# Optimization experiments

Measured on AMD Instinct MI355X. Metric: run time of the kernel, lower is better.

Reference implementation:

```python
import jax, jax.numpy as jnp
import numpy as np

EPS = 1e-5  # torch group_norm default
GROUPS = 32


def _nin(t, W, b):
    # torch Nin: einsum('bchw,co->bowh') transposes spatial dims, then adds bias
    return jnp.einsum('bchw,co->bowh', t, W) + b


def setup_inputs() -> dict:
    key = jax.random.key(0)
    ks = jax.random.split(key, 9)
    B, C, N = 16, 512, 32
    x = jax.random.normal(ks[0], (B, C, N, N), jnp.float32)
    sc = 0.02
    Wq = jax.random.normal(ks[1], (C, C), jnp.float32) * sc
    Wk = jax.random.normal(ks[2], (C, C), jnp.float32) * sc
    Wv = jax.random.normal(ks[3], (C, C), jnp.float32) * sc
    Wn = jax.random.normal(ks[4], (C, C), jnp.float32) * sc
    bq = jnp.zeros((1, C, 1, 1), jnp.float32)
    bk = jnp.zeros((1, C, 1, 1), jnp.float32)
    bv = jnp.zeros((1, C, 1, 1), jnp.float32)
    bn = jnp.zeros((1, C, 1, 1), jnp.float32)
    return {"x": x, "Wq": Wq, "bq": bq, "Wk": Wk, "bk": bk,
            "Wv": Wv, "bv": bv, "Wn": Wn, "bn": bn}


def reference(x, Wq, bq, Wk, bk, Wv, bv, Wn, bn):
    B, C, H, W = x.shape
    # GroupNorm(32) with no affine params
    xg = x.reshape(B, GROUPS, -1)
    mu = xg.mean(-1, keepdims=True)
    var = xg.var(-1, keepdims=True)
    h = ((xg - mu) / jnp.sqrt(var + EPS)).reshape(B, C, H, W)
    # Nin projections -> spatially transposed (B, C, W, H)
    q = _nin(h, Wq, bq)
    k = _nin(h, Wk, bk)
    v = _nin(h, Wv, bv)
    # scores s[b,w1,w2,h1,h2] = sum_c q[b,c,w1,h1] k[b,c,w2,h2] * C^-0.5
    s = jnp.einsum('bcwh,bcWH->bwWhH', q, k) * (C ** -0.5)
    # softmax over flat (h1,h2) blocks exactly as the torch reshape does
    s = jax.nn.softmax(s.reshape(B, H, W, H * W), axis=-1).reshape(B, H, W, H, W)
    # torch.einsum('bHWHW, bcWH -> bcWH', w, v) takes the DIAGONAL over the
    # repeated H and W labels: diag[b,i,j] = s[b,i,j,i,j], then elementwise
    # scales v: out[b,c,w,h] = diag[b,h,w] * v[b,c,w,h]
    i = jnp.arange(H)
    j = jnp.arange(W)
    diag = s[:, i[:, None], j[None, :], i[:, None], j[None, :]]  # (B,H,W)
    h2 = v * jnp.swapaxes(diag, 1, 2)[:, None]  # (B,C,W,H)
    out = _nin(h2, Wn, bn)  # transposes back -> (B,C,H,W)
    return x + out
```

## Files before the change

kernel.cpp:

```cpp
#include <hip/hip_runtime.h>
#include <hip/hip_bf16.h>

typedef __attribute__((ext_vector_type(8))) short short8;
typedef __attribute__((ext_vector_type(4))) float floatx4;

#define MFMA16(a, b, c) __builtin_amdgcn_mfma_f32_16x16x32_bf16((a), (b), (c), 0, 0, 0)

__device__ __forceinline__ short f2bf(float f) {
    union { float f; unsigned u; } x; x.f = f;
    unsigned r = (x.u + 0x7fffu + ((x.u >> 16) & 1u)) >> 16;
    return (short)r;
}

__device__ __forceinline__ void gl2lds16(const short* g, short* l) {
    void* gv = const_cast<short*>(g);
    __builtin_amdgcn_global_load_lds((__attribute__((address_space(1))) void*)gv,
                                     (__attribute__((address_space(3))) void*)l,
                                     16, 0, 0);
}

__global__ void transpose_w4(const float* __restrict__ Wq, const float* __restrict__ Wk,
                             const float* __restrict__ Wv, const float* __restrict__ Wn,
                             const float* __restrict__ bq, const float* __restrict__ bk,
                             const float* __restrict__ bv,
                             short* __restrict__ Wqkv_t, short* __restrict__ Wn_t,
                             float* __restrict__ bias_cat) {
    __shared__ float t[32][33];
    int z = blockIdx.z;
    const float* Wsrc = (z == 0) ? Wq : (z == 1) ? Wk : (z == 2) ? Wv : Wn;
    int o0 = blockIdx.x * 32, c0 = blockIdx.y * 32;
    int lx = threadIdx.x, ly = threadIdx.y;
    for (int i = ly; i < 32; i += 8) t[i][lx] = Wsrc[(size_t)(c0 + i) * 512 + o0 + lx];
    __syncthreads();
    for (int i = ly; i < 32; i += 8) {
        short v = f2bf(t[lx][i]);
        if (z < 3) Wqkv_t[(size_t)(z * 512 + o0 + i) * 512 + c0 + lx] = v;
        else       Wn_t[(size_t)(o0 + i) * 512 + c0 + lx] = v;
    }
    if (z < 3 && blockIdx.y == 0 && ly == 0) {
        const float* bsrc = (z == 0) ? bq : (z == 1) ? bk : bv;
        bias_cat[z * 512 + o0 + lx] = bsrc[o0 + lx];
    }
}

__global__ __launch_bounds__(256) void groupnorm_k(const float* __restrict__ x,
                                                   short* __restrict__ hnt) {
    int b = blockIdx.x >> 5, g = blockIdx.x & 31;
    const float* xg = x + ((size_t)b * 512 + g * 16) * 1024;
    const float4* xg4 = (const float4*)xg;
    float s = 0.f, ss = 0.f;
    for (int i = threadIdx.x; i < 4096; i += 256) {
        float4 v = xg4[i];
        s  += v.x + v.y + v.z + v.w;
        ss += v.x * v.x + v.y * v.y + v.z * v.z + v.w * v.w;
    }
#pragma unroll
    for (int off = 32; off > 0; off >>= 1) {
        s  += __shfl_down(s,  off, 64);
        ss += __shfl_down(ss, off, 64);
    }
    __shared__ float red[8];
    int w = threadIdx.x >> 6;
    if ((threadIdx.x & 63) == 0) { red[w] = s; red[4 + w] = ss; }
    __syncthreads();
    float S  = red[0] + red[1] + red[2] + red[3];
    float SS = red[4] + red[5] + red[6] + red[7];
    float mean = S * (1.f / 16384.f);
    float var  = SS * (1.f / 16384.f) - mean * mean;
    float rstd = rsqrtf(var + 1e-5f);
    __shared__ __attribute__((aligned(16))) short tile[16 * 1026];
    for (int i = threadIdx.x; i < 4096; i += 256) {
        float4 v = xg4[i];
        int c = i >> 8, p = (i & 255) * 4;
        short* tp = tile + c * 1026 + p;
        tp[0] = f2bf((v.x - mean) * rstd);
        tp[1] = f2bf((v.y - mean) * rstd);
        tp[2] = f2bf((v.z - mean) * rstd);
        tp[3] = f2bf((v.w - mean) * rstd);
    }
    __syncthreads();
    for (int i = threadIdx.x; i < 2048; i += 256) {
        int p = i >> 1, half = i & 1;
        short8 v;
#pragma unroll
        for (int j = 0; j < 8; ++j) v[j] = tile[(half * 8 + j) * 1026 + p];
        *(short8*)(hnt + ((size_t)b * 1024 + p) * 512 + g * 16 + half * 8) = v;
    }
}

__global__ __launch_bounds__(256) void qkv_gemm(const short* __restrict__ A,
                                                const short* __restrict__ Wt,
                                                const float* __restrict__ bias_cat,
                                                short* __restrict__ Qp,
                                                short* __restrict__ Kp,
                                                short* __restrict__ Vb) {
    const int tid = threadIdx.x;
    const int wv = tid >> 6, ln = tid & 63;
    const int m0 = blockIdx.x * 128, n0 = blockIdx.y * 128;
    const size_t BS = 1024 * 512;
    const short* Ab = A + (size_t)blockIdx.z * BS;
    const int tsel = n0 >> 9;
    const int permute = (tsel < 2);
    short* Ob = ((tsel == 0) ? Qp : (tsel == 1) ? Kp : Vb) + (size_t)blockIdx.z * BS;

    __shared__ __attribute__((aligned(16))) short As[128 * 32];
    __shared__ __attribute__((aligned(16))) short Bs[128 * 32];

    floatx4 acc[4][4] = {};
    const int wm = (wv >> 1) * 64, wn = (wv & 1) * 64;
    const int fr = ln & 15, fq = ln >> 4;

    for (int kk = 0; kk < 512; kk += 32) {
        __syncthreads();
#pragma unroll
        for (int j = 0; j < 2; ++j) {
            int s = (wv * 2 + j) * 64 + ln;
            int r = s >> 2;
            int q = (s & 3) ^ ((r >> 1) & 3);
            gl2lds16(Ab + (size_t)(m0 + r) * 512 + kk + q * 8, As + (size_t)(wv * 2 + j) * 512);
            gl2lds16(Wt + (size_t)(n0 + r) * 512 + kk + q * 8, Bs + (size_t)(wv * 2 + j) * 512);
        }
        __syncthreads();
        short8 af[4], bfr[4];
#pragma unroll
        for (int t = 0; t < 4; ++t) {
            int ra = wm + t * 16 + fr;
            af[t]  = *(const short8*)(As + ra * 32 + ((fq ^ ((ra >> 1) & 3)) * 8));
            int rb = wn + t * 16 + fr;
            bfr[t] = *(const short8*)(Bs + rb * 32 + ((fq ^ ((rb >> 1) & 3)) * 8));
        }
#pragma unroll
        for (int mt = 0; mt < 4; ++mt)
#pragma unroll
            for (int nt = 0; nt < 4; ++nt)
                acc[mt][nt] = MFMA16(af[mt], bfr[nt], acc[mt][nt]);
    }
#pragma unroll
    for (int mt = 0; mt < 4; ++mt) {
#pragma unroll
        for (int nt = 0; nt < 4; ++nt) {
            int n = n0 + wn + nt * 16 + fr;
            float bvv = bias_cat[n];
            int nn = n & 511;
#pragma unroll
            for (int r = 0; r < 4; ++r) {
                int m = m0 + wm + mt * 16 + fq * 4 + r;
                int mrow = permute ? ((m & 31) * 32 + (m >> 5)) : m;
                Ob[(size_t)mrow * 512 + nn] = f2bf(acc[mt][nt][r] + bvv);
            }
        }
    }
}

__global__ __launch_bounds__(256, 2) void attn_sm(const short* __restrict__ Qp,
                                                  const short* __restrict__ Kp,
                                                  float* __restrict__ Dm) {
    const int tid = threadIdx.x;
    const int wv = tid >> 6, ln = tid & 63;
    const int m0 = blockIdx.x * 128, n0 = blockIdx.y * 256, b = blockIdx.z;
    const short* Qb = Qp + (size_t)b * (1024 * 512);
    const short* Kb = Kp + (size_t)b * (1024 * 512);

    __shared__ __attribute__((aligned(16))) short As[128 * 32];
    __shared__ __attribute__((aligned(16))) short Bs[256 * 32];

    floatx4 acc[4][8] = {};
    const int wm = (wv >> 1) * 64, wn = (wv & 1) * 128;
    const int fr = ln & 15, fq = ln >> 4;

    for (int kk = 0; kk < 512; kk += 32) {
        __syncthreads();
#pragma unroll
        for (int j = 0; j < 2; ++j) {
            int s = (wv * 2 + j) * 64 + ln;
            int r = s >> 2;
            int q = (s & 3) ^ ((r >> 1) & 3);
            gl2lds16(Qb + (size_t)(m0 + r) * 512 + kk + q * 8, As + (size_t)(wv * 2 + j) * 512);
        }
#pragma unroll
        for (int j = 0; j < 4; ++j) {
            int s = (wv * 4 + j) * 64 + ln;
            int r = s >> 2;
            int q = (s & 3) ^ ((r >> 1) & 3);
            gl2lds16(Kb + (size_t)(n0 + r) * 512 + kk + q * 8, Bs + (size_t)(wv * 4 + j) * 512);
        }
        __syncthreads();
        short8 af[4], bfr[8];
#pragma unroll
        for (int t = 0; t < 4; ++t) {
            int ra = wm + t * 16 + fr;
            af[t] = *(const short8*)(As + ra * 32 + ((fq ^ ((ra >> 1) & 3)) * 8));
        }
#pragma unroll
        for (int u = 0; u < 8; ++u) {
            int rb = wn + u * 16 + fr;
            bfr[u] = *(const short8*)(Bs + rb * 32 + ((fq ^ ((rb >> 1) & 3)) * 8));
        }
#pragma unroll
        for (int mt = 0; mt < 4; ++mt)
#pragma unroll
            for (int nt = 0; nt < 8; ++nt)
                acc[mt][nt] = MFMA16(af[mt], bfr[nt], acc[mt][nt]);
    }

    const float scale = 0.04419417382415922f;
    const int wbase = (m0 + wm) >> 5;
    const int Wbase = (n0 + wn) >> 5;
#pragma unroll
    for (int si = 0; si < 2; ++si) {
#pragma unroll
        for (int sj = 0; sj < 4; ++sj) {
            int wg = wbase + si, Wg = Wbase + sj;
            float tv[16];
            float mx = -3.0e38f;
#pragma unroll
            for (int mi = 0; mi < 2; ++mi)
#pragma unroll
                for (int ni = 0; ni < 2; ++ni)
#pragma unroll
                    for (int r = 0; r < 4; ++r) {
                        float u = acc[2 * si + mi][2 * sj + ni][r] * scale;
                        tv[(mi * 2 + ni) * 4 + r] = u;
                        mx = fmaxf(mx, u);
                    }
#pragma unroll
            for (int off = 32; off > 0; off >>= 1) mx = fmaxf(mx, __shfl_xor(mx, off, 64));
            float se = 0.f;
#pragma unroll
            for (int i = 0; i < 16; ++i) se += __expf(tv[i] - mx);
#pragma unroll
            for (int off = 32; off > 0; off >>= 1) se += __shfl_xor(se, off, 64);
            if (fq == ((wg >> 2) & 3) && fr == (Wg & 15)) {
                int mi = wg >> 4, ni = Wg >> 4;
                float numer = tv[(mi * 2 + ni) * 4 + (wg & 3)];
                Dm[((size_t)b * 32 + wg) * 32 + Wg] = __expf(numer - mx) / se;
            }
        }
    }
}

__global__ __launch_bounds__(256) void out_gemm(const short* __restrict__ A,
                                                const short* __restrict__ Wt,
                                                const float* __restrict__ Dm,
                                                const float* __restrict__ bnb,
                                                const float* __restrict__ x,
                                                float* __restrict__ out) {
    const int tid = threadIdx.x;
    const int wv = tid >> 6, ln = tid & 63;
    const int m0 = blockIdx.x * 128, n0 = blockIdx.y * 128, b = blockIdx.z;
    const size_t BS = 1024 * 512;
    const short* Ab = A + (size_t)b * BS;

    __shared__ __attribute__((aligned(16))) short As[128 * 32];
    __shared__ __attribute__((aligned(16))) short Bs[128 * 32];

    floatx4 acc[4][4] = {};
    const int wm = (wv >> 1) * 64, wn = (wv & 1) * 64;
    const int fr = ln & 15, fq = ln >> 4;

    for (int kk = 0; kk < 512; kk += 32) {
        __syncthreads();
#pragma unroll
        for (int j = 0; j < 2; ++j) {
            int s = (wv * 2 + j) * 64 + ln;
            int r = s >> 2;
            int q = (s & 3) ^ ((r >> 1) & 3);
            gl2lds16(Ab + (size_t)(m0 + r) * 512 + kk + q * 8, As + (size_t)(wv * 2 + j) * 512);
            gl2lds16(Wt + (size_t)(n0 + r) * 512 + kk + q * 8, Bs + (size_t)(wv * 2 + j) * 512);
        }
        __syncthreads();
        short8 af[4], bfr[4];
#pragma unroll
        for (int t = 0; t < 4; ++t) {
            int ra = wm + t * 16 + fr;
            af[t]  = *(const short8*)(As + ra * 32 + ((fq ^ ((ra >> 1) & 3)) * 8));
            int rb = wn + t * 16 + fr;
            bfr[t] = *(const short8*)(Bs + rb * 32 + ((fq ^ ((rb >> 1) & 3)) * 8));
        }
#pragma unroll
        for (int mt = 0; mt < 4; ++mt)
#pragma unroll
            for (int nt = 0; nt < 4; ++nt)
                acc[mt][nt] = MFMA16(af[mt], bfr[nt], acc[mt][nt]);
    }
#pragma unroll
    for (int mt = 0; mt < 4; ++mt) {
        int mbase = m0 + wm + mt * 16 + fq * 4;
        float4 d4 = *(const float4*)(Dm + (size_t)b * 1024 + mbase);
#pragma unroll
        for (int nt = 0; nt < 4; ++nt) {
            int n = n0 + wn + nt * 16 + fr;
            float bvv = bnb[n];
            size_t base = ((size_t)b * 512 + n) * 1024 + mbase;
            float4 x4 = *(const float4*)(x + base);
            float4 o;
            o.x = x4.x + d4.x * acc[mt][nt][0] + bvv;
            o.y = x4.y + d4.y * acc[mt][nt][1] + bvv;
            o.z = x4.z + d4.z * acc[mt][nt][2] + bvv;
            o.w = x4.w + d4.w * acc[mt][nt][3] + bvv;
            *(float4*)(out + base) = o;
        }
    }
}

extern "C" void kernel_launch(void* const* d_in, const int* in_sizes, int n_in,
                              void* d_out, int out_size, void* d_ws, size_t ws_size,
                              hipStream_t stream) {
    const float* x  = (const float*)d_in[0];
    const float* Wq = (const float*)d_in[1];
    const float* bq = (const float*)d_in[2];
    const float* Wk = (const float*)d_in[3];
    const float* bk = (const float*)d_in[4];
    const float* Wv = (const float*)d_in[5];
    const float* bv = (const float*)d_in[6];
    const float* Wn = (const float*)d_in[7];
    const float* bn = (const float*)d_in[8];
    float* out = (float*)d_out;
    char* ws = (char*)d_ws;

    const size_t WQKV = (size_t)1536 * 512 * 2;
    const size_t WSZ  = (size_t)512 * 512 * 2;
    const size_t BIAS = 1536 * sizeof(float);
    const size_t TSZ  = (size_t)16 * 1024 * 512 * 2;
    short* Wqkv_t   = (short*)(ws);
    short* Wn_t     = (short*)(ws + WQKV);
    float* bias_cat = (float*)(ws + WQKV + WSZ);
    char*  base     = ws + WQKV + WSZ + BIAS;
    short* hnt = (short*)(base);
    short* Qp  = (short*)(base + TSZ);
    short* Kp  = (short*)(base + 2 * TSZ);
    short* Vb  = (short*)(base + 3 * TSZ);
    float* Dm  = (float*)(base + 4 * TSZ);

    transpose_w4<<<dim3(16, 16, 4), dim3(32, 8), 0, stream>>>(
        Wq, Wk, Wv, Wn, bq, bk, bv, Wqkv_t, Wn_t, bias_cat);
    groupnorm_k<<<512, 256, 0, stream>>>(x, hnt);
    qkv_gemm<<<dim3(8, 12, 16), 256, 0, stream>>>(hnt, Wqkv_t, bias_cat, Qp, Kp, Vb);
    attn_sm<<<dim3(8, 4, 16), 256, 0, stream>>>(Qp, Kp, Dm);
    out_gemm<<<dim3(8, 4, 16), 256, 0, stream>>>(Vb, Wn_t, Dm, bn, x, out);
}
```

Baseline: 209.7 us.

## Double-buffer LDS tiles in all three GEMM kernels to overlap loads with MFMA

```diff
diff --git a/kernel.cpp b/kernel.cpp
--- a/kernel.cpp
+++ b/kernel.cpp
@@ -103,37 +103,53 @@
     const int permute = (tsel < 2);
     short* Ob = ((tsel == 0) ? Qp : (tsel == 1) ? Kp : Vb) + (size_t)blockIdx.z * BS;
 
-    __shared__ __attribute__((aligned(16))) short As[128 * 32];
-    __shared__ __attribute__((aligned(16))) short Bs[128 * 32];
+    __shared__ __attribute__((aligned(16))) short As[2][128 * 32];
+    __shared__ __attribute__((aligned(16))) short Bs[2][128 * 32];
 
     floatx4 acc[4][4] = {};
     const int wm = (wv >> 1) * 64, wn = (wv & 1) * 64;
     const int fr = ln & 15, fq = ln >> 4;
 
+    int sr[2], sq[2];
+#pragma unroll
+    for (int j = 0; j < 2; ++j) {
+        int s = (wv * 2 + j) * 64 + ln;
+        sr[j] = s >> 2;
+        sq[j] = ((s & 3) ^ ((sr[j] >> 1) & 3)) * 8;
+    }
+
+#pragma unroll
+    for (int j = 0; j < 2; ++j) {
+        gl2lds16(Ab + (size_t)(m0 + sr[j]) * 512 + sq[j], &As[0][(wv * 2 + j) * 512]);
+        gl2lds16(Wt + (size_t)(n0 + sr[j]) * 512 + sq[j], &Bs[0][(wv * 2 + j) * 512]);
+    }
+    __syncthreads();
+
+    int cur = 0;
     for (int kk = 0; kk < 512; kk += 32) {
-        __syncthreads();
-#pragma unroll
-        for (int j = 0; j < 2; ++j) {
-            int s = (wv * 2 + j) * 64 + ln;
-            int r = s >> 2;
-            int q = (s & 3) ^ ((r >> 1) & 3);
-            gl2lds16(Ab + (size_t)(m0 + r) * 512 + kk + q * 8, As + (size_t)(wv * 2 + j) * 512);
-            gl2lds16(Wt + (size_t)(n0 + r) * 512 + kk + q * 8, Bs + (size_t)(wv * 2 + j) * 512);
-        }
-        __syncthreads();
+        if (kk < 480) {
+            int nxt = cur ^ 1;
+#pragma unroll
+            for (int j = 0; j < 2; ++j) {
+                gl2lds16(Ab + (size_t)(m0 + sr[j]) * 512 + kk + 32 + sq[j], &As[nxt][(wv * 2 + j) * 512]);
+                gl2lds16(Wt + (size_t)(n0 + sr[j]) * 512 + kk + 32 + sq[j], &Bs[nxt][(wv * 2 + j) * 512]);
+            }
+        }
         short8 af[4], bfr[4];
 #pragma unroll
         for (int t = 0; t < 4; ++t) {
             int ra = wm + t * 16 + fr;
-            af[t]  = *(const short8*)(As + ra * 32 + ((fq ^ ((ra >> 1) & 3)) * 8));
+            af[t]  = *(const short8*)(&As[cur][ra * 32 + ((fq ^ ((ra >> 1) & 3)) * 8)]);
             int rb = wn + t * 16 + fr;
-            bfr[t] = *(const short8*)(Bs + rb * 32 + ((fq ^ ((rb >> 1) & 3)) * 8));
+            bfr[t] = *(const short8*)(&Bs[cur][rb * 32 + ((fq ^ ((rb >> 1) & 3)) * 8)]);
         }
 #pragma unroll
         for (int mt = 0; mt < 4; ++mt)
 #pragma unroll
             for (int nt = 0; nt < 4; ++nt)
                 acc[mt][nt] = MFMA16(af[mt], bfr[nt], acc[mt][nt]);
+        __syncthreads();
+        cur ^= 1;
     }
 #pragma unroll
     for (int mt = 0; mt < 4; ++mt) {
@@ -161,46 +177,64 @@
     const short* Qb = Qp + (size_t)b * (1024 * 512);
     const short* Kb = Kp + (size_t)b * (1024 * 512);
 
-    __shared__ __attribute__((aligned(16))) short As[128 * 32];
-    __shared__ __attribute__((aligned(16))) short Bs[256 * 32];
+    __shared__ __attribute__((aligned(16))) short As[2][128 * 32];
+    __shared__ __attribute__((aligned(16))) short Bs[2][256 * 32];
 
     floatx4 acc[4][8] = {};
     const int wm = (wv >> 1) * 64, wn = (wv & 1) * 128;
     const int fr = ln & 15, fq = ln >> 4;
 
+    int ar[2], aq[2], br[4], bq_[4];
+#pragma unroll
+    for (int j = 0; j < 2; ++j) {
+        int s = (wv * 2 + j) * 64 + ln;
+        ar[j] = s >> 2;
+        aq[j] = ((s & 3) ^ ((ar[j] >> 1) & 3)) * 8;
+    }
+#pragma unroll
+    for (int j = 0; j < 4; ++j) {
+        int s = (wv * 4 + j) * 64 + ln;
+        br[j] = s >> 2;
+        bq_[j] = ((s & 3) ^ ((br[j] >> 1) & 3)) * 8;
+    }
+
+#pragma unroll
+    for (int j = 0; j < 2; ++j)
+        gl2lds16(Qb + (size_t)(m0 + ar[j]) * 512 + aq[j], &As[0][(wv * 2 + j) * 512]);
+#pragma unroll
+    for (int j = 0; j < 4; ++j)
+        gl2lds16(Kb + (size_t)(n0 + br[j]) * 512 + bq_[j], &Bs[0][(wv * 4 + j) * 512]);
+    __syncthreads();
+
+    int cur = 0;
     for (int kk = 0; kk < 512; kk += 32) {
-        __syncthreads();
-#pragma unroll
-        for (int j = 0; j < 2; ++j) {
-            int s = (wv * 2 + j) * 64 + ln;
-            int r = s >> 2;
-            int q = (s & 3) ^ ((r >> 1) & 3);
-            gl2lds16(Qb + (size_t)(m0 + r) * 512 + kk + q * 8, As + (size_t)(wv * 2 + j) * 512);
-        }
-#pragma unroll
-        for (int j = 0; j < 4; ++j) {
-            int s = (wv * 4 + j) * 64 + ln;
-            int r = s >> 2;
-            int q = (s & 3) ^ ((r >> 1) & 3);
-            gl2lds16(Kb + (size_t)(n0 + r) * 512 + kk + q * 8, Bs + (size_t)(wv * 4 + j) * 512);
-        }
-        __syncthreads();
+        if (kk < 480) {
+            int nxt = cur ^ 1;
+#pragma unroll
+            for (int j = 0; j < 2; ++j)
+                gl2lds16(Qb + (size_t)(m0 + ar[j]) * 512 + kk + 32 + aq[j], &As[nxt][(wv * 2 + j) * 512]);
+#pragma unroll
+            for (int j = 0; j < 4; ++j)
+                gl2lds16(Kb + (size_t)(n0 + br[j]) * 512 + kk + 32 + bq_[j], &Bs[nxt][(wv * 4 + j) * 512]);
+        }
         short8 af[4], bfr[8];
 #pragma unroll
         for (int t = 0; t < 4; ++t) {
             int ra = wm + t * 16 + fr;
-            af[t] = *(const short8*)(As + ra * 32 + ((fq ^ ((ra >> 1) & 3)) * 8));
+            af[t] = *(const short8*)(&As[cur][ra * 32 + ((fq ^ ((ra >> 1) & 3)) * 8)]);
         }
 #pragma unroll
         for (int u = 0; u < 8; ++u) {
             int rb = wn + u * 16 + fr;
-            bfr[u] = *(const short8*)(Bs + rb * 32 + ((fq ^ ((rb >> 1) & 3)) * 8));
+            bfr[u] = *(const short8*)(&Bs[cur][rb * 32 + ((fq ^ ((rb >> 1) & 3)) * 8)]);
         }
 #pragma unroll
         for (int mt = 0; mt < 4; ++mt)
 #pragma unroll
             for (int nt = 0; nt < 8; ++nt)
                 acc[mt][nt] = MFMA16(af[mt], bfr[nt], acc[mt][nt]);
+        __syncthreads();
+        cur ^= 1;
     }
 
     const float scale = 0.04419417382415922f;
@@ -251,37 +285,53 @@
     const size_t BS = 1024 * 512;
     const short* Ab = A + (size_t)b * BS;
 
-    __shared__ __attribute__((aligned(16))) short As[128 * 32];
-    __shared__ __attribute__((aligned(16))) short Bs[128 * 32];
+    __shared__ __attribute__((aligned(16))) short As[2][128 * 32];
+    __shared__ __attribute__((aligned(16))) short Bs[2][128 * 32];
 
     floatx4 acc[4][4] = {};
     const int wm = (wv >> 1) * 64, wn = (wv & 1) * 64;
     const int fr = ln & 15, fq = ln >> 4;
 
+    int sr[2], sq[2];
+#pragma unroll
+    for (int j = 0; j < 2; ++j) {
+        int s = (wv * 2 + j) * 64 + ln;
+        sr[j] = s >> 2;
+        sq[j] = ((s & 3) ^ ((sr[j] >> 1) & 3)) * 8;
+    }
+
+#pragma unroll
+    for (int j = 0; j < 2; ++j) {
+        gl2lds16(Ab + (size_t)(m0 + sr[j]) * 512 + sq[j], &As[0][(wv * 2 + j) * 512]);
+        gl2lds16(Wt + (size_t)(n0 + sr[j]) * 512 + sq[j], &Bs[0][(wv * 2 + j) * 512]);
+    }
+    __syncthreads();
+
+    int cur = 0;
     for (int kk = 0; kk < 512; kk += 32) {
-        __syncthreads();
-#pragma unroll
-        for (int j = 0; j < 2; ++j) {
-            int s = (wv * 2 + j) * 64 + ln;
-            int r = s >> 2;
-            int q = (s & 3) ^ ((r >> 1) & 3);
-            gl2lds16(Ab + (size_t)(m0 + r) * 512 + kk + q * 8, As + (size_t)(wv * 2 + j) * 512);
-            gl2lds16(Wt + (size_t)(n0 + r) * 512 + kk + q * 8, Bs + (size_t)(wv * 2 + j) * 512);
-        }
-        __syncthreads();
+        if (kk < 480) {
+            int nxt = cur ^ 1;
+#pragma unroll
+            for (int j = 0; j < 2; ++j) {
+                gl2lds16(Ab + (size_t)(m0 + sr[j]) * 512 + kk + 32 + sq[j], &As[nxt][(wv * 2 + j) * 512]);
+                gl2lds16(Wt + (size_t)(n0 + sr[j]) * 512 + kk + 32 + sq[j], &Bs[nxt][(wv * 2 + j) * 512]);
+            }
+        }
         short8 af[4], bfr[4];
 #pragma unroll
         for (int t = 0; t < 4; ++t) {
             int ra = wm + t * 16 + fr;
-            af[t]  = *(const short8*)(As + ra * 32 + ((fq ^ ((ra >> 1) & 3)) * 8));
+            af[t]  = *(const short8*)(&As[cur][ra * 32 + ((fq ^ ((ra >> 1) & 3)) * 8)]);
             int rb = wn + t * 16 + fr;
-            bfr[t] = *(const short8*)(Bs + rb * 32 + ((fq ^ ((rb >> 1) & 3)) * 8));
+            bfr[t] = *(const short8*)(&Bs[cur][rb * 32 + ((fq ^ ((rb >> 1) & 3)) * 8)]);
         }
 #pragma unroll
         for (int mt = 0; mt < 4; ++mt)
 #pragma unroll
             for (int nt = 0; nt < 4; ++nt)
                 acc[mt][nt] = MFMA16(af[mt], bfr[nt], acc[mt][nt]);
+        __syncthreads();
+        cur ^= 1;
     }
 #pragma unroll
     for (int mt = 0; mt < 4; ++mt) {
```

New measurement: 210.7 us. About the same (+0.5%).

## Use 256x256 double-buffered pipelined GEMM tiles with XCD-aware block mapping

Applied to the files above, without the earlier changes.

```diff
diff --git a/kernel.cpp b/kernel.cpp
--- a/kernel.cpp
+++ b/kernel.cpp
@@ -5,6 +5,8 @@
 typedef __attribute__((ext_vector_type(4))) float floatx4;
 
 #define MFMA16(a, b, c) __builtin_amdgcn_mfma_f32_16x16x32_bf16((a), (b), (c), 0, 0, 0)
+#define WAIT_VM(N) asm volatile("s_waitcnt vmcnt(" #N ")" ::: "memory")
+#define BARM() do { asm volatile("" ::: "memory"); __builtin_amdgcn_s_barrier(); asm volatile("" ::: "memory"); } while (0)
 
 __device__ __forceinline__ short f2bf(float f) {
     union { float f; unsigned u; } x; x.f = f;
@@ -88,128 +90,217 @@
     }
 }
 
-__global__ __launch_bounds__(256) void qkv_gemm(const short* __restrict__ A,
-                                                const short* __restrict__ Wt,
-                                                const float* __restrict__ bias_cat,
-                                                short* __restrict__ Qp,
-                                                short* __restrict__ Kp,
-                                                short* __restrict__ Vb) {
+
+__global__ __launch_bounds__(512, 2) void qkv_gemm256(const short* __restrict__ A,
+                                                      const short* __restrict__ Wt,
+                                                      const float* __restrict__ bias_cat,
+                                                      short* __restrict__ Qp,
+                                                      short* __restrict__ Kp,
+                                                      short* __restrict__ Vb) {
     const int tid = threadIdx.x;
-    const int wv = tid >> 6, ln = tid & 63;
-    const int m0 = blockIdx.x * 128, n0 = blockIdx.y * 128;
-    const size_t BS = 1024 * 512;
-    const short* Ab = A + (size_t)blockIdx.z * BS;
+    const int wid = tid >> 6, ln = tid & 63;
+    const int wrow = wid >> 2, wcol = wid & 3;
+    const int fid = blockIdx.x;
+    const int xcd = fid & 7, s = fid >> 3;
+    const int mt = xcd * 8 + s / 6, nt = s % 6;
+    const int m0 = mt * 256, n0 = nt * 256;
     const int tsel = n0 >> 9;
     const int permute = (tsel < 2);
-    short* Ob = ((tsel == 0) ? Qp : (tsel == 1) ? Kp : Vb) + (size_t)blockIdx.z * BS;
-
-    __shared__ __attribute__((aligned(16))) short As[128 * 32];
-    __shared__ __attribute__((aligned(16))) short Bs[128 * 32];
-
-    floatx4 acc[4][4] = {};
-    const int wm = (wv >> 1) * 64, wn = (wv & 1) * 64;
+    short* Ob = (tsel == 0) ? Qp : (tsel == 1) ? Kp : Vb;
+
+    __shared__ __attribute__((aligned(16))) short Asb[2][256 * 64];
+    __shared__ __attribute__((aligned(16))) short Bsb[2][256 * 64];
+
+    floatx4 acc[8][4] = {};
     const int fr = ln & 15, fq = ln >> 4;
 
-    for (int kk = 0; kk < 512; kk += 32) {
-        __syncthreads();
-#pragma unroll
-        for (int j = 0; j < 2; ++j) {
-            int s = (wv * 2 + j) * 64 + ln;
-            int r = s >> 2;
-            int q = (s & 3) ^ ((r >> 1) & 3);
-            gl2lds16(Ab + (size_t)(m0 + r) * 512 + kk + q * 8, As + (size_t)(wv * 2 + j) * 512);
-            gl2lds16(Wt + (size_t)(n0 + r) * 512 + kk + q * 8, Bs + (size_t)(wv * 2 + j) * 512);
-        }
-        __syncthreads();
-        short8 af[4], bfr[4];
+    const int srow = wid * 8 + (ln >> 3);
+    const int schk = (ln & 7) ^ ((ln >> 3) & 7);
+    const short* gA = A + (size_t)(m0 + srow) * 512 + schk * 8;
+    const short* gB = Wt + (size_t)(n0 + srow) * 512 + schk * 8;
+
+    short* Ac = &Asb[0][0]; short* Bc = &Bsb[0][0];
+    short* An = &Asb[1][0]; short* Bn = &Bsb[1][0];
+
+    auto SA = [&](int j, short* db) { gl2lds16(gA + (size_t)j * 32768, db + j * 4096 + wid * 512); };
+    auto SB = [&](int j, short* db) { gl2lds16(gB + (size_t)j * 32768, db + j * 4096 + wid * 512); };
+    auto LDA = [&](const short* Ap, int mh, int ks, short8* dst) {
 #pragma unroll
         for (int t = 0; t < 4; ++t) {
-            int ra = wm + t * 16 + fr;
-            af[t]  = *(const short8*)(As + ra * 32 + ((fq ^ ((ra >> 1) & 3)) * 8));
-            int rb = wn + t * 16 + fr;
-            bfr[t] = *(const short8*)(Bs + rb * 32 + ((fq ^ ((rb >> 1) & 3)) * 8));
-        }
-#pragma unroll
-        for (int mt = 0; mt < 4; ++mt)
-#pragma unroll
-            for (int nt = 0; nt < 4; ++nt)
-                acc[mt][nt] = MFMA16(af[mt], bfr[nt], acc[mt][nt]);
-    }
-#pragma unroll
-    for (int mt = 0; mt < 4; ++mt) {
-#pragma unroll
-        for (int nt = 0; nt < 4; ++nt) {
-            int n = n0 + wn + nt * 16 + fr;
+            int ra = wrow * 128 + (mh * 4 + t) * 16 + fr;
+            dst[t] = *(const short8*)(Ap + ra * 64 + (((ks << 2) | fq) ^ (fr & 7)) * 8);
+        }
+    };
+    auto LDB = [&](const short* Bp, int ks, short8* dst) {
+#pragma unroll
+        for (int nf = 0; nf < 4; ++nf) {
+            int rb = wcol * 64 + nf * 16 + fr;
+            dst[nf] = *(const short8*)(Bp + rb * 64 + (((ks << 2) | fq) ^ (fr & 7)) * 8);
+        }
+    };
+    auto MM = [&](int mh, const short8* a_, const short8* b_) {
+        __builtin_amdgcn_s_setprio(1);
+#pragma unroll
+        for (int t = 0; t < 4; ++t)
+#pragma unroll
+            for (int nf = 0; nf < 4; ++nf)
+                acc[mh * 4 + t][nf] = MFMA16(a_[t], b_[nf], acc[mh * 4 + t][nf]);
+        __builtin_amdgcn_s_setprio(0);
+    };
+
+    SA(0, Ac); SA(2, Ac); SB(0, Bc); SB(1, Bc); SB(2, Bc); SB(3, Bc); SA(1, Ac); SA(3, Ac);
+    gA += 64; gB += 64;
+    WAIT_VM(2);
+    BARM();
+
+    short8 a_[4], p0[4], p1[4];
+    for (int kt = 0; kt < 8; ++kt) {
+        const bool st = (kt < 7);
+        LDA(Ac, 0, 0, a_); LDB(Bc, 0, p0);
+        if (st) { SA(0, An); SA(2, An); }
+        BARM();
+        MM(0, a_, p0);
+        BARM();
+        LDA(Ac, 0, 1, a_); LDB(Bc, 1, p1);
+        if (st) { SB(0, Bn); SB(1, Bn); }
+        BARM();
+        MM(0, a_, p1);
+        if (st) { WAIT_VM(4); } else { WAIT_VM(0); }
+        BARM();
+        LDA(Ac, 1, 0, a_);
+        if (st) { SB(2, Bn); SB(3, Bn); }
+        BARM();
+        MM(1, a_, p0);
+        BARM();
+        LDA(Ac, 1, 1, a_);
+        if (st) { SA(1, An); SA(3, An); }
+        BARM();
+        MM(1, a_, p1);
+        if (st) { WAIT_VM(2); }
+        BARM();
+        short* t0 = Ac; Ac = An; An = t0;
+        short* t1 = Bc; Bc = Bn; Bn = t1;
+        if (st) { gA += 64; gB += 64; }
+    }
+
+    const size_t BS = 1024 * 512;
+#pragma unroll
+    for (int mf = 0; mf < 8; ++mf) {
+        int m = m0 + wrow * 128 + mf * 16 + fq * 4;
+        int batch = m >> 10;
+        short* Obb = Ob + (size_t)batch * BS;
+#pragma unroll
+        for (int nf = 0; nf < 4; ++nf) {
+            int n = n0 + wcol * 64 + nf * 16 + fr;
             float bvv = bias_cat[n];
             int nn = n & 511;
 #pragma unroll
             for (int r = 0; r < 4; ++r) {
-                int m = m0 + wm + mt * 16 + fq * 4 + r;
-                int mrow = permute ? ((m & 31) * 32 + (m >> 5)) : m;
-                Ob[(size_t)mrow * 512 + nn] = f2bf(acc[mt][nt][r] + bvv);
+                int p = (m + r) & 1023;
+                int mrow = permute ? ((p & 31) * 32 + (p >> 5)) : p;
+                Obb[(size_t)mrow * 512 + nn] = f2bf(acc[mf][nf][r] + bvv);
             }
         }
     }
 }
 
-__global__ __launch_bounds__(256, 2) void attn_sm(const short* __restrict__ Qp,
-                                                  const short* __restrict__ Kp,
-                                                  float* __restrict__ Dm) {
+__global__ __launch_bounds__(512, 2) void attn_sm256(const short* __restrict__ Qp,
+                                                     const short* __restrict__ Kp,
+                                                     float* __restrict__ Dm) {
     const int tid = threadIdx.x;
-    const int wv = tid >> 6, ln = tid & 63;
-    const int m0 = blockIdx.x * 128, n0 = blockIdx.y * 256, b = blockIdx.z;
-    const short* Qb = Qp + (size_t)b * (1024 * 512);
-    const short* Kb = Kp + (size_t)b * (1024 * 512);
-
-    __shared__ __attribute__((aligned(16))) short As[128 * 32];
-    __shared__ __attribute__((aligned(16))) short Bs[256 * 32];
-
-    floatx4 acc[4][8] = {};
-    const int wm = (wv >> 1) * 64, wn = (wv & 1) * 128;
+    const int wid = tid >> 6, ln = tid & 63;
+    const int wrow = wid >> 2, wcol = wid & 3;
+    const int fid = blockIdx.x;
+    const int xcd = fid & 7, slot = fid >> 3;
+    const int b = xcd * 2 + (slot >> 4);
+    const int t4 = slot & 15;
+    const int m0 = (t4 & 3) * 256, n0 = (t4 >> 2) * 256;
+    const size_t BS = 1024 * 512;
+    const short* Qb = Qp + (size_t)b * BS;
+    const short* Kb = Kp + (size_t)b * BS;
+
+    __shared__ __attribute__((aligned(16))) short Asb[2][256 * 64];
+    __shared__ __attribute__((aligned(16))) short Bsb[2][256 * 64];
+
+    floatx4 acc[8][4] = {};
     const int fr = ln & 15, fq = ln >> 4;
 
-    for (int kk = 0; kk < 512; kk += 32) {
-        __syncthreads();
-#pragma unroll
-        for (int j = 0; j < 2; ++j) {
-            int s = (wv * 2 + j) * 64 + ln;
-            int r = s >> 2;
-            int q = (s & 3) ^ ((r >> 1) & 3);
-            gl2lds16(Qb + (size_t)(m0 + r) * 512 + kk + q * 8, As + (size_t)(wv * 2 + j) * 512);
-        }
-#pragma unroll
-        for (int j = 0; j < 4; ++j) {
-            int s = (wv * 4 + j) * 64 + ln;
-            int r = s >> 2;
-            int q = (s & 3) ^ ((r >> 1) & 3);
-            gl2lds16(Kb + (size_t)(n0 + r) * 512 + kk + q * 8, Bs + (size_t)(wv * 4 + j) * 512);
-        }
-        __syncthreads();
-        short8 af[4], bfr[8];
+    const int srow = wid * 8 + (ln >> 3);
+    const int schk = (ln & 7) ^ ((ln >> 3) & 7);
+    const short* gA = Qb + (size_t)(m0 + srow) * 512 + schk * 8;
+    const short* gB = Kb + (size_t)(n0 + srow) * 512 + schk * 8;
+
+    short* Ac = &Asb[0][0]; short* Bc = &Bsb[0][0];
+    short* An = &Asb[1][0]; short* Bn = &Bsb[1][0];
+
+    auto SA = [&](int j, short* db) { gl2lds16(gA + (size_t)j * 32768, db + j * 4096 + wid * 512); };
+    auto SB = [&](int j, short* db) { gl2lds16(gB + (size_t)j * 32768, db + j * 4096 + wid * 512); };
+    auto LDA = [&](const short* Ap, int mh, int ks, short8* dst) {
 #pragma unroll
         for (int t = 0; t < 4; ++t) {
-            int ra = wm + t * 16 + fr;
-            af[t] = *(const short8*)(As + ra * 32 + ((fq ^ ((ra >> 1) & 3)) * 8));
-        }
-#pragma unroll
-        for (int u = 0; u < 8; ++u) {
-            int rb = wn + u * 16 + fr;
-            bfr[u] = *(const short8*)(Bs + rb * 32 + ((fq ^ ((rb >> 1) & 3)) * 8));
-        }
-#pragma unroll
-        for (int mt = 0; mt < 4; ++mt)
-#pragma unroll
-            for (int nt = 0; nt < 8; ++nt)
-                acc[mt][nt] = MFMA16(af[mt], bfr[nt], acc[mt][nt]);
+            int ra = wrow * 128 + (mh * 4 + t) * 16 + fr;
+            dst[t] = *(const short8*)(Ap + ra * 64 + (((ks << 2) | fq) ^ (fr & 7)) * 8);
+        }
+    };
+    auto LDB = [&](const short* Bp, int ks, short8* dst) {
+#pragma unroll
+        for (int nf = 0; nf < 4; ++nf) {
+            int rb = wcol * 64 + nf * 16 + fr;
+            dst[nf] = *(const short8*)(Bp + rb * 64 + (((ks << 2) | fq) ^ (fr & 7)) * 8);
+        }
+    };
+    auto MM = [&](int mh, const short8* a_, const short8* b_) {
+        __builtin_amdgcn_s_setprio(1);
+#pragma unroll
+        for (int t = 0; t < 4; ++t)
+#pragma unroll
+            for (int nf = 0; nf < 4; ++nf)
+                acc[mh * 4 + t][nf] = MFMA16(a_[t], b_[nf], acc[mh * 4 + t][nf]);
+        __builtin_amdgcn_s_setprio(0);
+    };
+
+    SA(0, Ac); SA(2, Ac); SB(0, Bc); SB(1, Bc); SB(2, Bc); SB(3, Bc); SA(1, Ac); SA(3, Ac);
+    gA += 64; gB += 64;
+    WAIT_VM(2);
+    BARM();
+
+    short8 a_[4], p0[4], p1[4];
+    for (int kt = 0; kt < 8; ++kt) {
+        const bool st = (kt < 7);
+        LDA(Ac, 0, 0, a_); LDB(Bc, 0, p0);
+        if (st) { SA(0, An); SA(2, An); }
+        BARM();
+        MM(0, a_, p0);
+        BARM();
+        LDA(Ac, 0, 1, a_); LDB(Bc, 1, p1);
+        if (st) { SB(0, Bn); SB(1, Bn); }
+        BARM();
+        MM(0, a_, p1);
+        if (st) { WAIT_VM(4); } else { WAIT_VM(0); }
+        BARM();
+        LDA(Ac, 1, 0, a_);
+        if (st) { SB(2, Bn); SB(3, Bn); }
+        BARM();
+        MM(1, a_, p0);
+        BARM();
+        LDA(Ac, 1, 1, a_);
+        if (st) { SA(1, An); SA(3, An); }
+        BARM();
+        MM(1, a_, p1);
+        if (st) { WAIT_VM(2); }
+        BARM();
+        short* t0 = Ac; Ac = An; An = t0;
+        short* t1 = Bc; Bc = Bn; Bn = t1;
+        if (st) { gA += 64; gB += 64; }
     }
 
     const float scale = 0.04419417382415922f;
-    const int wbase = (m0 + wm) >> 5;
-    const int Wbase = (n0 + wn) >> 5;
-#pragma unroll
-    for (int si = 0; si < 2; ++si) {
-#pragma unroll
-        for (int sj = 0; sj < 4; ++sj) {
+    const int wbase = (m0 + wrow * 128) >> 5;
+    const int Wbase = (n0 + wcol * 64) >> 5;
+#pragma unroll
+    for (int si = 0; si < 4; ++si) {
+#pragma unroll
+        for (int sj = 0; sj < 2; ++sj) {
             int wg = wbase + si, Wg = Wbase + sj;
             float tv[16];
             float mx = -3.0e38f;
@@ -247,42 +338,82 @@
                                                 float* __restrict__ out) {
     const int tid = threadIdx.x;
     const int wv = tid >> 6, ln = tid & 63;
-    const int m0 = blockIdx.x * 128, n0 = blockIdx.y * 128, b = blockIdx.z;
+    const int fid = blockIdx.x + (blockIdx.y << 3) + blockIdx.z * 32;
+    const int xcd = fid & 7, slot = fid >> 3;
+    const int bb = (slot >= 32) ? 1 : 0;
+    const int w = slot - bb * 32;
+    const int b = xcd * 2 + bb;
+    const int m0 = (w & 7) * 128, n0 = (w >> 3) * 128;
     const size_t BS = 1024 * 512;
     const short* Ab = A + (size_t)b * BS;
 
-    __shared__ __attribute__((aligned(16))) short As[128 * 32];
-    __shared__ __attribute__((aligned(16))) short Bs[128 * 32];
+    __shared__ __attribute__((aligned(16))) short As[3][128 * 32];
+    __shared__ __attribute__((aligned(16))) short Bs[3][128 * 32];
 
     floatx4 acc[4][4] = {};
     const int wm = (wv >> 1) * 64, wn = (wv & 1) * 64;
     const int fr = ln & 15, fq = ln >> 4;
 
-    for (int kk = 0; kk < 512; kk += 32) {
-        __syncthreads();
-#pragma unroll
-        for (int j = 0; j < 2; ++j) {
-            int s = (wv * 2 + j) * 64 + ln;
-            int r = s >> 2;
-            int q = (s & 3) ^ ((r >> 1) & 3);
-            gl2lds16(Ab + (size_t)(m0 + r) * 512 + kk + q * 8, As + (size_t)(wv * 2 + j) * 512);
-            gl2lds16(Wt + (size_t)(n0 + r) * 512 + kk + q * 8, Bs + (size_t)(wv * 2 + j) * 512);
-        }
-        __syncthreads();
+    int sr[2], sq[2];
+#pragma unroll
+    for (int j = 0; j < 2; ++j) {
+        int s = (wv * 2 + j) * 64 + ln;
+        sr[j] = s >> 2;
+        sq[j] = ((s & 3) ^ ((sr[j] >> 1) & 3)) * 8;
+    }
+    int aoff[4], boff[4];
+#pragma unroll
+    for (int t = 0; t < 4; ++t) {
+        int ra = wm + t * 16 + fr;
+        aoff[t] = ra * 32 + ((fq ^ ((ra >> 1) & 3)) * 8);
+        int rb = wn + t * 16 + fr;
+        boff[t] = rb * 32 + ((fq ^ ((rb >> 1) & 3)) * 8);
+    }
+
+    short* a0 = &As[0][0]; short* a1 = &As[1][0]; short* a2 = &As[2][0];
+    short* b0 = &Bs[0][0]; short* b1 = &Bs[1][0]; short* b2 = &Bs[2][0];
+
+#pragma unroll
+    for (int j = 0; j < 2; ++j) {
+        gl2lds16(Ab + (size_t)(m0 + sr[j]) * 512 + sq[j],      a0 + (wv * 2 + j) * 512);
+        gl2lds16(Wt + (size_t)(n0 + sr[j]) * 512 + sq[j],      b0 + (wv * 2 + j) * 512);
+        gl2lds16(Ab + (size_t)(m0 + sr[j]) * 512 + 32 + sq[j], a1 + (wv * 2 + j) * 512);
+        gl2lds16(Wt + (size_t)(n0 + sr[j]) * 512 + 32 + sq[j], b1 + (wv * 2 + j) * 512);
+    }
+
+    auto compute = [&](const short* Ap, const short* Bp) {
         short8 af[4], bfr[4];
 #pragma unroll
         for (int t = 0; t < 4; ++t) {
-            int ra = wm + t * 16 + fr;
-            af[t]  = *(const short8*)(As + ra * 32 + ((fq ^ ((ra >> 1) & 3)) * 8));
-            int rb = wn + t * 16 + fr;
-            bfr[t] = *(const short8*)(Bs + rb * 32 + ((fq ^ ((rb >> 1) & 3)) * 8));
+            af[t]  = *(const short8*)(Ap + aoff[t]);
+            bfr[t] = *(const short8*)(Bp + boff[t]);
         }
 #pragma unroll
         for (int mt = 0; mt < 4; ++mt)
 #pragma unroll
             for (int nt = 0; nt < 4; ++nt)
                 acc[mt][nt] = MFMA16(af[mt], bfr[nt], acc[mt][nt]);
-    }
+    };
+
+    for (int t = 0; t < 14; ++t) {
+        int kp = t * 32 + 64;
+#pragma unroll
+        for (int j = 0; j < 2; ++j) {
+            gl2lds16(Ab + (size_t)(m0 + sr[j]) * 512 + kp + sq[j], a2 + (wv * 2 + j) * 512);
+            gl2lds16(Wt + (size_t)(n0 + sr[j]) * 512 + kp + sq[j], b2 + (wv * 2 + j) * 512);
+        }
+        WAIT_VM(8);
+        BARM();
+        compute(a0, b0);
+        BARM();
+        short* ta = a0; a0 = a1; a1 = a2; a2 = ta;
+        short* tb = b0; b0 = b1; b1 = b2; b2 = tb;
+    }
+    WAIT_VM(4); BARM();
+    compute(a0, b0);
+    WAIT_VM(0); BARM();
+    compute(a1, b1);
+
 #pragma unroll
     for (int mt = 0; mt < 4; ++mt) {
         int mbase = m0 + wm + mt * 16 + fq * 4;
@@ -335,7 +466,7 @@
     transpose_w4<<<dim3(16, 16, 4), dim3(32, 8), 0, stream>>>(
         Wq, Wk, Wv, Wn, bq, bk, bv, Wqkv_t, Wn_t, bias_cat);
     groupnorm_k<<<512, 256, 0, stream>>>(x, hnt);
-    qkv_gemm<<<dim3(8, 12, 16), 256, 0, stream>>>(hnt, Wqkv_t, bias_cat, Qp, Kp, Vb);
-    attn_sm<<<dim3(8, 4, 16), 256, 0, stream>>>(Qp, Kp, Dm);
+    qkv_gemm256<<<384, 512, 0, stream>>>(hnt, Wqkv_t, bias_cat, Qp, Kp, Vb);
+    attn_sm256<<<256, 512, 0, stream>>>(Qp, Kp, Dm);
     out_gemm<<<dim3(8, 4, 16), 256, 0, stream>>>(Vb, Wn_t, Dm, bn, x, out);
 }
```

Result: faster. 199.3 us (-5.0%).

## Restructure GEMMs to stage full-K A tile in LDS and stream B from global

Applied to the files above, without the earlier changes.

```diff
diff --git a/kernel.cpp b/kernel.cpp
--- a/kernel.cpp
+++ b/kernel.cpp
@@ -88,128 +88,146 @@
     }
 }
 
-__global__ __launch_bounds__(256) void qkv_gemm(const short* __restrict__ A,
-                                                const short* __restrict__ Wt,
-                                                const float* __restrict__ bias_cat,
-                                                short* __restrict__ Qp,
-                                                short* __restrict__ Kp,
-                                                short* __restrict__ Vb) {
+
+__global__ __launch_bounds__(512, 2) void qkv_fk(const short* __restrict__ A,
+                                                 const short* __restrict__ Wt,
+                                                 const float* __restrict__ bias_cat,
+                                                 short* __restrict__ Qp,
+                                                 short* __restrict__ Kp,
+                                                 short* __restrict__ Vb) {
     const int tid = threadIdx.x;
-    const int wv = tid >> 6, ln = tid & 63;
-    const int m0 = blockIdx.x * 128, n0 = blockIdx.y * 128;
-    const size_t BS = 1024 * 512;
-    const short* Ab = A + (size_t)blockIdx.z * BS;
+    const int wid = tid >> 6, ln = tid & 63;
+    const int wrow = wid >> 2, wcol = wid & 3;
+    const int fr = ln & 15, fq = ln >> 4, fr7 = fr & 7;
+    const int fid = blockIdx.x;
+    const int xcd = fid & 7, s = fid >> 3;
+    const int m0 = (xcd * 16 + s / 6) * 128, n0 = (s % 6) * 256;
     const int tsel = n0 >> 9;
     const int permute = (tsel < 2);
-    short* Ob = ((tsel == 0) ? Qp : (tsel == 1) ? Kp : Vb) + (size_t)blockIdx.z * BS;
-
-    __shared__ __attribute__((aligned(16))) short As[128 * 32];
-    __shared__ __attribute__((aligned(16))) short Bs[128 * 32];
+    short* Ob = (tsel == 0) ? Qp : (tsel == 1) ? Kp : Vb;
+
+    __shared__ __attribute__((aligned(16))) short Alds[128 * 512];
+
+#pragma unroll
+    for (int j = 0; j < 16; ++j) {
+        int r = wid * 16 + j;
+        gl2lds16(A + (size_t)(m0 + r) * 512 + ((ln ^ (j & 7)) * 8), Alds + r * 512);
+    }
 
     floatx4 acc[4][4] = {};
-    const int wm = (wv >> 1) * 64, wn = (wv & 1) * 64;
-    const int fr = ln & 15, fq = ln >> 4;
-
-    for (int kk = 0; kk < 512; kk += 32) {
-        __syncthreads();
-#pragma unroll
-        for (int j = 0; j < 2; ++j) {
-            int s = (wv * 2 + j) * 64 + ln;
-            int r = s >> 2;
-            int q = (s & 3) ^ ((r >> 1) & 3);
-            gl2lds16(Ab + (size_t)(m0 + r) * 512 + kk + q * 8, As + (size_t)(wv * 2 + j) * 512);
-            gl2lds16(Wt + (size_t)(n0 + r) * 512 + kk + q * 8, Bs + (size_t)(wv * 2 + j) * 512);
-        }
-        __syncthreads();
-        short8 af[4], bfr[4];
-#pragma unroll
-        for (int t = 0; t < 4; ++t) {
-            int ra = wm + t * 16 + fr;
-            af[t]  = *(const short8*)(As + ra * 32 + ((fq ^ ((ra >> 1) & 3)) * 8));
-            int rb = wn + t * 16 + fr;
-            bfr[t] = *(const short8*)(Bs + rb * 32 + ((fq ^ ((rb >> 1) & 3)) * 8));
-        }
-#pragma unroll
-        for (int mt = 0; mt < 4; ++mt)
-#pragma unroll
-            for (int nt = 0; nt < 4; ++nt)
-                acc[mt][nt] = MFMA16(af[mt], bfr[nt], acc[mt][nt]);
-    }
+    const short* lB = Wt + (size_t)(n0 + wcol * 64 + fr) * 512 + fq * 8;
+    const short* lA = Alds + (wrow * 64 + fr) * 512;
+
+    short8 bc[4], bn_[4], af[4];
+#pragma unroll
+    for (int nf = 0; nf < 4; ++nf) bc[nf] = *(const short8*)(lB + nf * 8192);
+
+    __syncthreads();
+
+#pragma unroll
+    for (int t = 0; t < 16; ++t) {
+#pragma unroll
+        for (int mt = 0; mt < 4; ++mt)
+            af[mt] = *(const short8*)(lA + mt * 8192 + ((((t << 2) | fq) ^ fr7) * 8));
+        if (t < 15) {
+#pragma unroll
+            for (int nf = 0; nf < 4; ++nf)
+                bn_[nf] = *(const short8*)(lB + nf * 8192 + t * 32 + 32);
+        }
+#pragma unroll
+        for (int mt = 0; mt < 4; ++mt)
+#pragma unroll
+            for (int nf = 0; nf < 4; ++nf)
+                acc[mt][nf] = MFMA16(af[mt], bc[nf], acc[mt][nf]);
+        if (t < 15) {
+#pragma unroll
+            for (int nf = 0; nf < 4; ++nf) bc[nf] = bn_[nf];
+        }
+    }
+
+    const size_t BS = 1024 * 512;
+    const int batch = m0 >> 10;
+    short* Obb = Ob + (size_t)batch * BS;
 #pragma unroll
     for (int mt = 0; mt < 4; ++mt) {
-#pragma unroll
-        for (int nt = 0; nt < 4; ++nt) {
-            int n = n0 + wn + nt * 16 + fr;
+        int m = m0 + wrow * 64 + mt * 16 + fq * 4;
+#pragma unroll
+        for (int nf = 0; nf < 4; ++nf) {
+            int n = n0 + wcol * 64 + nf * 16 + fr;
             float bvv = bias_cat[n];
             int nn = n & 511;
 #pragma unroll
             for (int r = 0; r < 4; ++r) {
-                int m = m0 + wm + mt * 16 + fq * 4 + r;
-                int mrow = permute ? ((m & 31) * 32 + (m >> 5)) : m;
-                Ob[(size_t)mrow * 512 + nn] = f2bf(acc[mt][nt][r] + bvv);
+                int p = (m + r) & 1023;
+                int mrow = permute ? ((p & 31) * 32 + (p >> 5)) : p;
+                Obb[(size_t)mrow * 512 + nn] = f2bf(acc[mt][nf][r] + bvv);
             }
         }
     }
 }
 
-__global__ __launch_bounds__(256, 2) void attn_sm(const short* __restrict__ Qp,
+__global__ __launch_bounds__(512, 2) void attn_fk(const short* __restrict__ Qp,
                                                   const short* __restrict__ Kp,
                                                   float* __restrict__ Dm) {
     const int tid = threadIdx.x;
-    const int wv = tid >> 6, ln = tid & 63;
-    const int m0 = blockIdx.x * 128, n0 = blockIdx.y * 256, b = blockIdx.z;
-    const short* Qb = Qp + (size_t)b * (1024 * 512);
-    const short* Kb = Kp + (size_t)b * (1024 * 512);
-
-    __shared__ __attribute__((aligned(16))) short As[128 * 32];
-    __shared__ __attribute__((aligned(16))) short Bs[256 * 32];
-
-    floatx4 acc[4][8] = {};
-    const int wm = (wv >> 1) * 64, wn = (wv & 1) * 128;
-    const int fr = ln & 15, fq = ln >> 4;
-
-    for (int kk = 0; kk < 512; kk += 32) {
-        __syncthreads();
-#pragma unroll
-        for (int j = 0; j < 2; ++j) {
-            int s = (wv * 2 + j) * 64 + ln;
-            int r = s >> 2;
-            int q = (s & 3) ^ ((r >> 1) & 3);
-            gl2lds16(Qb + (size_t)(m0 + r) * 512 + kk + q * 8, As + (size_t)(wv * 2 + j) * 512);
-        }
-#pragma unroll
-        for (int j = 0; j < 4; ++j) {
-            int s = (wv * 4 + j) * 64 + ln;
-            int r = s >> 2;
-            int q = (s & 3) ^ ((r >> 1) & 3);
-            gl2lds16(Kb + (size_t)(n0 + r) * 512 + kk + q * 8, Bs + (size_t)(wv * 4 + j) * 512);
-        }
-        __syncthreads();
-        short8 af[4], bfr[8];
-#pragma unroll
-        for (int t = 0; t < 4; ++t) {
-            int ra = wm + t * 16 + fr;
-            af[t] = *(const short8*)(As + ra * 32 + ((fq ^ ((ra >> 1) & 3)) * 8));
-        }
-#pragma unroll
-        for (int u = 0; u < 8; ++u) {
-            int rb = wn + u * 16 + fr;
-            bfr[u] = *(const short8*)(Bs + rb * 32 + ((fq ^ ((rb >> 1) & 3)) * 8));
-        }
-#pragma unroll
-        for (int mt = 0; mt < 4; ++mt)
-#pragma unroll
-            for (int nt = 0; nt < 8; ++nt)
-                acc[mt][nt] = MFMA16(af[mt], bfr[nt], acc[mt][nt]);
+    const int wid = tid >> 6, ln = tid & 63;
+    const int wrow = wid >> 2, wcol = wid & 3;
+    const int fr = ln & 15, fq = ln >> 4, fr7 = fr & 7;
+    const int fid = blockIdx.x;
+    const int xcd = fid & 7, slot = fid >> 3;
+    const int b = xcd * 2 + (slot >> 5);
+    const int inner = slot & 31;
+    const int m0 = (inner & 7) * 128, n0 = (inner >> 3) * 256;
+    const size_t BS = 1024 * 512;
+    const short* Qb = Qp + (size_t)b * BS;
+    const short* Kb = Kp + (size_t)b * BS;
+
+    __shared__ __attribute__((aligned(16))) short Alds[128 * 512];
+
+#pragma unroll
+    for (int j = 0; j < 16; ++j) {
+        int r = wid * 16 + j;
+        gl2lds16(Qb + (size_t)(m0 + r) * 512 + ((ln ^ (j & 7)) * 8), Alds + r * 512);
+    }
+
+    floatx4 acc[4][4] = {};
+    const short* lB = Kb + (size_t)(n0 + wcol * 64 + fr) * 512 + fq * 8;
+    const short* lA = Alds + (wrow * 64 + fr) * 512;
+
+    short8 bc[4], bn_[4], af[4];
+#pragma unroll
+    for (int nf = 0; nf < 4; ++nf) bc[nf] = *(const short8*)(lB + nf * 8192);
+
+    __syncthreads();
+
+#pragma unroll
+    for (int t = 0; t < 16; ++t) {
+#pragma unroll
+        for (int mt = 0; mt < 4; ++mt)
+            af[mt] = *(const short8*)(lA + mt * 8192 + ((((t << 2) | fq) ^ fr7) * 8));
+        if (t < 15) {
+#pragma unroll
+            for (int nf = 0; nf < 4; ++nf)
+                bn_[nf] = *(const short8*)(lB + nf * 8192 + t * 32 + 32);
+        }
+#pragma unroll
+        for (int mt = 0; mt < 4; ++mt)
+#pragma unroll
+            for (int nf = 0; nf < 4; ++nf)
+                acc[mt][nf] = MFMA16(af[mt], bc[nf], acc[mt][nf]);
+        if (t < 15) {
+#pragma unroll
+            for (int nf = 0; nf < 4; ++nf) bc[nf] = bn_[nf];
+        }
     }
 
     const float scale = 0.04419417382415922f;
-    const int wbase = (m0 + wm) >> 5;
-    const int Wbase = (n0 + wn) >> 5;
+    const int wbase = (m0 + wrow * 64) >> 5;
+    const int Wbase = (n0 + wcol * 64) >> 5;
 #pragma unroll
     for (int si = 0; si < 2; ++si) {
 #pragma unroll
-        for (int sj = 0; sj < 4; ++sj) {
+        for (int sj = 0; sj < 2; ++sj) {
             int wg = wbase + si, Wg = Wbase + sj;
             float tv[16];
             float mx = -3.0e38f;
@@ -239,65 +257,78 @@
     }
 }
 
-__global__ __launch_bounds__(256) void out_gemm(const short* __restrict__ A,
-                                                const short* __restrict__ Wt,
-                                                const float* __restrict__ Dm,
-                                                const float* __restrict__ bnb,
-                                                const float* __restrict__ x,
-                                                float* __restrict__ out) {
+__global__ __launch_bounds__(512, 2) void out_fk(const short* __restrict__ A,
+                                                 const short* __restrict__ Wt,
+                                                 const float* __restrict__ Dm,
+                                                 const float* __restrict__ bnb,
+                                                 const float* __restrict__ x,
+                                                 float* __restrict__ out) {
     const int tid = threadIdx.x;
-    const int wv = tid >> 6, ln = tid & 63;
-    const int m0 = blockIdx.x * 128, n0 = blockIdx.y * 128, b = blockIdx.z;
+    const int wid = tid >> 6, ln = tid & 63;
+    const int wrow = wid >> 2, wcol = wid & 3;
+    const int fr = ln & 15, fq = ln >> 4, fr7 = fr & 7;
+    const int fid = blockIdx.x;
+    const int xcd = fid & 7, slot = fid >> 3;
+    const int b = xcd * 2 + (slot >> 4);
+    const int inner = slot & 15;
+    const int m0 = (inner & 7) * 128, n0 = (inner >> 3) * 256;
     const size_t BS = 1024 * 512;
     const short* Ab = A + (size_t)b * BS;
 
-    __shared__ __attribute__((aligned(16))) short As[128 * 32];
-    __shared__ __attribute__((aligned(16))) short Bs[128 * 32];
+    __shared__ __attribute__((aligned(16))) short Alds[128 * 512];
+
+#pragma unroll
+    for (int j = 0; j < 16; ++j) {
+        int r = wid * 16 + j;
+        gl2lds16(Ab + (size_t)(m0 + r) * 512 + ((ln ^ (j & 7)) * 8), Alds + r * 512);
+    }
 
     floatx4 acc[4][4] = {};
-    const int wm = (wv >> 1) * 64, wn = (wv & 1) * 64;
-    const int fr = ln & 15, fq = ln >> 4;
-
-    for (int kk = 0; kk < 512; kk += 32) {
-        __syncthreads();
-#pragma unroll
-        for (int j = 0; j < 2; ++j) {
-            int s = (wv * 2 + j) * 64 + ln;
-            int r = s >> 2;
-            int q = (s & 3) ^ ((r >> 1) & 3);
-            gl2lds16(Ab + (size_t)(m0 + r) * 512 + kk + q * 8, As + (size_t)(wv * 2 + j) * 512);
-            gl2lds16(Wt + (size_t)(n0 + r) * 512 + kk + q * 8, Bs + (size_t)(wv * 2 + j) * 512);
-        }
-        __syncthreads();
-        short8 af[4], bfr[4];
-#pragma unroll
-        for (int t = 0; t < 4; ++t) {
-            int ra = wm + t * 16 + fr;
-            af[t]  = *(const short8*)(As + ra * 32 + ((fq ^ ((ra >> 1) & 3)) * 8));
-            int rb = wn + t * 16 + fr;
-            bfr[t] = *(const short8*)(Bs + rb * 32 + ((fq ^ ((rb >> 1) & 3)) * 8));
-        }
-#pragma unroll
-        for (int mt = 0; mt < 4; ++mt)
-#pragma unroll
-            for (int nt = 0; nt < 4; ++nt)
-                acc[mt][nt] = MFMA16(af[mt], bfr[nt], acc[mt][nt]);
-    }
+    const short* lB = Wt + (size_t)(n0 + wcol * 64 + fr) * 512 + fq * 8;
+    const short* lA = Alds + (wrow * 64 + fr) * 512;
+
+    short8 bc[4], bn_[4], af[4];
+#pragma unroll
+    for (int nf = 0; nf < 4; ++nf) bc[nf] = *(const short8*)(lB + nf * 8192);
+
+    __syncthreads();
+
+#pragma unroll
+    for (int t = 0; t < 16; ++t) {
+#pragma unroll
+        for (int mt = 0; mt < 4; ++mt)
+            af[mt] = *(const short8*)(lA + mt * 8192 + ((((t << 2) | fq) ^ fr7) * 8));
+        if (t < 15) {
+#pragma unroll
+            for (int nf = 0; nf < 4; ++nf)
+                bn_[nf] = *(const short8*)(lB + nf * 8192 + t * 32 + 32);
+        }
+#pragma unroll
+        for (int mt = 0; mt < 4; ++mt)
+#pragma unroll
+            for (int nf = 0; nf < 4; ++nf)
+                acc[mt][nf] = MFMA16(af[mt], bc[nf], acc[mt][nf]);
+        if (t < 15) {
+#pragma unroll
+            for (int nf = 0; nf < 4; ++nf) bc[nf] = bn_[nf];
+        }
+    }
+
 #pragma unroll
     for (int mt = 0; mt < 4; ++mt) {
-        int mbase = m0 + wm + mt * 16 + fq * 4;
+        int mbase = m0 + wrow * 64 + mt * 16 + fq * 4;
         float4 d4 = *(const float4*)(Dm + (size_t)b * 1024 + mbase);
 #pragma unroll
-        for (int nt = 0; nt < 4; ++nt) {
-            int n = n0 + wn + nt * 16 + fr;
+        for (int nf = 0; nf < 4; ++nf) {
+            int n = n0 + wcol * 64 + nf * 16 + fr;
             float bvv = bnb[n];
             size_t base = ((size_t)b * 512 + n) * 1024 + mbase;
             float4 x4 = *(const float4*)(x + base);
             float4 o;
-            o.x = x4.x + d4.x * acc[mt][nt][0] + bvv;
-            o.y = x4.y + d4.y * acc[mt][nt][1] + bvv;
-            o.z = x4.z + d4.z * acc[mt][nt][2] + bvv;
-            o.w = x4.w + d4.w * acc[mt][nt][3] + bvv;
+            o.x = x4.x + d4.x * acc[mt][nf][0] + bvv;
+            o.y = x4.y + d4.y * acc[mt][nf][1] + bvv;
+            o.z = x4.z + d4.z * acc[mt][nf][2] + bvv;
+            o.w = x4.w + d4.w * acc[mt][nf][3] + bvv;
             *(float4*)(out + base) = o;
         }
     }
@@ -335,7 +366,7 @@
     transpose_w4<<<dim3(16, 16, 4), dim3(32, 8), 0, stream>>>(
         Wq, Wk, Wv, Wn, bq, bk, bv, Wqkv_t, Wn_t, bias_cat);
     groupnorm_k<<<512, 256, 0, stream>>>(x, hnt);
-    qkv_gemm<<<dim3(8, 12, 16), 256, 0, stream>>>(hnt, Wqkv_t, bias_cat, Qp, Kp, Vb);
-    attn_sm<<<dim3(8, 4, 16), 256, 0, stream>>>(Qp, Kp, Dm);
-    out_gemm<<<dim3(8, 4, 16), 256, 0, stream>>>(Vb, Wn_t, Dm, bn, x, out);
-}
+    qkv_fk<<<768, 512, 0, stream>>>(hnt, Wqkv_t, bias_cat, Qp, Kp, Vb);
+    attn_fk<<<512, 512, 0, stream>>>(Qp, Kp, Dm);
+    out_fk<<<256, 512, 0, stream>>>(Vb, Wn_t, Dm, bn, x, out);
+}
```

Result: slower. 246.5 us (+17.6%).
